# Kernel tuning notes

Hardware: AMD Instinct MI355X
Metric: run time of the kernel (lower is better)

The kernel has to match this reference:

```python
import jax, jax.numpy as jnp
import numpy as np

N, E, D = 100000, 1600000, 128
BN_EPS = 1e-5


def setup_inputs() -> dict:
    key = jax.random.key(0)
    k0, k1, k2 = jax.random.split(key, 3)
    x = jax.random.normal(k0, (N, D), dtype=jnp.float32)
    edge_index = jax.random.randint(k1, (2, E), 0, N, dtype=jnp.int32)
    # GCNConv weight (glorot-ish scale) and bias
    W = jax.random.normal(k2, (D, D), dtype=jnp.float32) * (1.0 / np.sqrt(D))
    b = jnp.zeros((D,), dtype=jnp.float32)
    # BatchNorm1d affine params
    gamma = jnp.ones((D,), dtype=jnp.float32)
    beta = jnp.zeros((D,), dtype=jnp.float32)
    # PReLU single shared slope (torch default init 0.25)
    a_prelu = jnp.asarray(0.25, dtype=jnp.float32)
    return {"x": x, "W": W, "b": b, "gamma": gamma, "beta": beta,
            "a_prelu": a_prelu, "edge_index": edge_index}


def reference(x, W, b, gamma, beta, a_prelu, edge_index):
    n = x.shape[0]
    loops = jnp.arange(n, dtype=edge_index.dtype)
    src = jnp.concatenate([edge_index[0], loops])  # [E+N]
    dst = jnp.concatenate([edge_index[1], loops])  # [E+N]

    # GCN symmetric normalization with self-loops: deg counts incoming edges
    deg = jax.ops.segment_sum(jnp.ones_like(dst, dtype=x.dtype), dst, num_segments=n)
    dinv = jax.lax.rsqrt(deg)  # deg >= 1 thanks to self-loops
    enorm = dinv[src] * dinv[dst]  # [E+N]

    xw = x @ W                                        # [N, D] transform first
    msg = xw[src] * enorm[:, None]                    # gather + scale
    out = jax.ops.segment_sum(msg, dst, num_segments=n) + b  # scatter-add

    # BatchNorm1d over nodes (training-mode batch statistics, biased var)
    mean = jnp.mean(out, axis=0)
    var = jnp.mean(jnp.square(out - mean), axis=0)
    out = (out - mean) * jax.lax.rsqrt(var + BN_EPS) * gamma + beta

    # PReLU (single shared slope); dropout is identity in eval mode
    out = jnp.where(out > 0, out, a_prelu * out)

    # identity residual (in_dim == out_dim)
    return out + x
```

## Files before the change

### kernel.cpp

```cpp
#include <hip/hip_runtime.h>

#define DIM 128
#define BSH 8
#define BUCK 256
#define CAP 6144
#define BINCH 1024
#define MAXB 1024
#define FPT 12

typedef __attribute__((ext_vector_type(8))) short bf16x8;
typedef __attribute__((ext_vector_type(4))) float f32x4;
union U8 { uint4 u; bf16x8 b; };

static __device__ __forceinline__ unsigned f2bf_bits(float f) {
  unsigned u = __float_as_uint(f);
  return (u + 0x7fffu + ((u >> 16) & 1u)) >> 16;
}
static __device__ __forceinline__ unsigned packbf(float a, float b) {
  return (f2bf_bits(a) & 0xffffu) | (f2bf_bits(b) << 16);
}
static __device__ __forceinline__ float bfu_lo(unsigned pk) { return __uint_as_float(pk << 16); }
static __device__ __forceinline__ float bfu_hi(unsigned pk) { return __uint_as_float(pk & 0xffff0000u); }

static __device__ __forceinline__ int eread(const int* __restrict__ e, long long idx, int fl64) {
  return fl64 ? e[idx * 2] : e[idx];
}

__global__ void k_probe(const int* __restrict__ eidx, int* __restrict__ iflag) {
  int lane = threadIdx.x;
  int w = eidx[lane * 2 + 1];
  unsigned long long m = __ballot(w == 0);
  if (lane == 0) *iflag = (__popcll(m) >= 48) ? 1 : 0;
}

__global__ __launch_bounds__(256) void k_prep(const int* __restrict__ eidx, int E,
                                              const int* __restrict__ iflag,
                                              int* __restrict__ bcnt,
                                              unsigned* __restrict__ tmp, int nbuck,
                                              const float* __restrict__ W,
                                              unsigned* __restrict__ wbt,
                                              int NBB) {
  __shared__ int hist[MAXB];
  __shared__ int lcur[MAXB];
  int bid = blockIdx.x;
  int tid = threadIdx.x;

  if (bid < NBB) {
    int fl = *iflag;
    long long ebase = (long long)bid * BINCH;
    for (int i = tid; i < nbuck; i += 256) hist[i] = 0;
    __syncthreads();
    unsigned pk[BINCH / 256];
    int bb[BINCH / 256];
#pragma unroll
    for (int it = 0; it < BINCH / 256; ++it) {
      long long e = ebase + it * 256 + tid;
      bb[it] = -1;
      if (e < E) {
        int s = eread(eidx, e, fl);
        int d = eread(eidx, (long long)E + e, fl);
        bb[it] = d >> BSH;
        pk[it] = ((unsigned)s << BSH) | (unsigned)(d & (BUCK - 1));
        atomicAdd(&hist[bb[it]], 1);
      }
    }
    __syncthreads();
    for (int b = tid; b < nbuck; b += 256) {
      int h = hist[b];
      lcur[b] = h ? atomicAdd(&bcnt[b], h) : 0;
    }
    __syncthreads();
#pragma unroll
    for (int it = 0; it < BINCH / 256; ++it) {
      if (bb[it] >= 0) {
        int sl = atomicAdd(&lcur[bb[it]], 1);
        if (sl < CAP) tmp[(unsigned)bb[it] * CAP + sl] = pk[it];
      }
    }
  } else {
    int w = (bid - NBB) * 256 + tid;
    int c = w >> 6, kk = w & 63;
    float lo = W[(unsigned)(2 * kk) * DIM + c];
    float hi = W[(unsigned)(2 * kk + 1) * DIM + c];
    wbt[(unsigned)c * 64 + kk] = packbf(lo, hi);
  }
}

__global__ __launch_bounds__(512) void k_fine(const int* __restrict__ bcnt,
                                              unsigned* __restrict__ tmp,
                                              int* __restrict__ ofs2,
                                              int* __restrict__ deg,
                                              float* __restrict__ dinv, int n) {
  __shared__ unsigned srt[CAP];
  __shared__ int hist[BUCK];
  __shared__ int sc[BUCK];
  __shared__ int lcur[BUCK];
  int b = blockIdx.x, tid = threadIdx.x;
  int cnt = bcnt[b];
  if (cnt > CAP) cnt = CAP;
  unsigned base = (unsigned)b * CAP;
  if (tid < BUCK) hist[tid] = 0;
  __syncthreads();
  unsigned r[FPT];
#pragma unroll
  for (int u = 0; u < FPT; ++u) {
    int j = u * 512 + tid;
    r[u] = 0xffffffffu;
    if (j < cnt) {
      r[u] = tmp[base + j];
      atomicAdd(&hist[r[u] & (BUCK - 1)], 1);
    }
  }
  __syncthreads();
  if (tid < 64) {
    int h0 = hist[tid * 4], h1 = hist[tid * 4 + 1];
    int h2 = hist[tid * 4 + 2], h3 = hist[tid * 4 + 3];
    int s = h0 + h1 + h2 + h3;
    int pre = s;
#pragma unroll
    for (int d = 1; d < 64; d <<= 1) {
      int t = __shfl_up(pre, d);
      if (tid >= d) pre += t;
    }
    pre -= s;
    int e0 = pre, e1 = pre + h0, e2 = e1 + h1, e3 = e2 + h2;
    sc[tid * 4] = e0;     lcur[tid * 4] = e0;
    sc[tid * 4 + 1] = e1; lcur[tid * 4 + 1] = e1;
    sc[tid * 4 + 2] = e2; lcur[tid * 4 + 2] = e2;
    sc[tid * 4 + 3] = e3; lcur[tid * 4 + 3] = e3;
  }
  __syncthreads();
#pragma unroll
  for (int u = 0; u < FPT; ++u) {
    if (r[u] != 0xffffffffu) {
      int sl = atomicAdd(&lcur[r[u] & (BUCK - 1)], 1);
      srt[sl] = r[u];
    }
  }
  __syncthreads();
#pragma unroll
  for (int u = 0; u < FPT; ++u) {
    int j = u * 512 + tid;
    if (j < cnt) tmp[base + j] = srt[j];
  }
  if (tid < BUCK) {
    int node = b * BUCK + tid;
    if (node < n) {
      int v = hist[tid];
      ofs2[node] = (int)base + sc[tid];
      deg[node] = v;
      dinv[node] = rsqrtf((float)(v + 1));
    }
  }
}

__global__ __launch_bounds__(256) void k_pack(const float* __restrict__ x,
                                              const float* __restrict__ dinv,
                                              unsigned* __restrict__ xb, int n) {
  int t = blockIdx.x * 256 + threadIdx.x;
  int i = t >> 6, p = t & 63;
  if (i >= n) return;
  float di = dinv[i];
  float2 v = *(const float2*)(x + (size_t)i * DIM + p * 2);
  xb[(unsigned)i * 64 + p] = packbf(v.x * di, v.y * di);
}

__global__ __launch_bounds__(256) void k_agg(const unsigned* __restrict__ xb,
                                             const unsigned* __restrict__ tmp,
                                             const int* __restrict__ ofs2,
                                             const int* __restrict__ deg,
                                             const float* __restrict__ dinv,
                                             unsigned* __restrict__ agg, int n) {
  int wid = blockIdx.x * 4 + (threadIdx.x >> 6);
  int lane = threadIdx.x & 63;
  if (wid >= n) return;
  float di = dinv[wid];
  unsigned xp = xb[(unsigned)wid * 64 + lane];
  float ax = bfu_lo(xp), ay = bfu_hi(xp);
  int e = __builtin_amdgcn_readfirstlane(ofs2[wid]);
  int e1 = e + __builtin_amdgcn_readfirstlane(deg[wid]);
  for (; e + 16 <= e1; e += 16) {
    unsigned s[16];
#pragma unroll
    for (int u = 0; u < 16; ++u) s[u] = tmp[(unsigned)(e + u)] >> BSH;
    unsigned v[16];
#pragma unroll
    for (int u = 0; u < 16; ++u) v[u] = xb[s[u] * 64 + lane];
#pragma unroll
    for (int u = 0; u < 16; ++u) { ax += bfu_lo(v[u]); ay += bfu_hi(v[u]); }
  }
  for (; e + 4 <= e1; e += 4) {
    unsigned s0 = tmp[(unsigned)e] >> BSH, s1 = tmp[(unsigned)e + 1] >> BSH;
    unsigned s2 = tmp[(unsigned)e + 2] >> BSH, s3 = tmp[(unsigned)e + 3] >> BSH;
    unsigned v0 = xb[s0 * 64 + lane], v1 = xb[s1 * 64 + lane];
    unsigned v2 = xb[s2 * 64 + lane], v3 = xb[s3 * 64 + lane];
    ax += bfu_lo(v0); ay += bfu_hi(v0);
    ax += bfu_lo(v1); ay += bfu_hi(v1);
    ax += bfu_lo(v2); ay += bfu_hi(v2);
    ax += bfu_lo(v3); ay += bfu_hi(v3);
  }
  for (; e < e1; ++e) {
    unsigned vv = xb[(tmp[(unsigned)e] >> BSH) * 64 + lane];
    ax += bfu_lo(vv); ay += bfu_hi(vv);
  }
  agg[(unsigned)wid * 64 + lane] = packbf(ax * di, ay * di);
}

__global__ __launch_bounds__(256) void k_gemm(
    const unsigned* __restrict__ agg, const unsigned* __restrict__ wbt,
    const float* __restrict__ bias, unsigned* __restrict__ preb,
    float* __restrict__ part, int n) {
  __shared__ unsigned SM[64 * 68 + 128 * 68];
  unsigned* As2 = SM;
  unsigned* WsT = SM + 64 * 68;
  int tid = threadIdx.x;
  int base = blockIdx.x * 64;

#pragma unroll
  for (int it = 0; it < 32; ++it) {
    int idx = it * 256 + tid;
    int c = idx >> 6, kk = idx & 63;
    WsT[c * 68 + kk] = wbt[idx];
  }
#pragma unroll
  for (int it = 0; it < 16; ++it) {
    int idx = it * 256 + tid;
    int rl = idx >> 6, c2 = idx & 63;
    int g = base + rl; if (g >= n) g = n - 1;
    As2[rl * 68 + c2] = agg[(unsigned)g * 64 + c2];
  }
  __syncthreads();

  int w = tid >> 6, l = tid & 63;
  int lg = l >> 4, lr = l & 15;
  f32x4 acc[8];
#pragma unroll
  for (int nt = 0; nt < 8; ++nt) acc[nt] = (f32x4){0.f, 0.f, 0.f, 0.f};

#pragma unroll
  for (int kt = 0; kt < 4; ++kt) {
    U8 bfr;
    bfr.u = *(const uint4*)&As2[(w * 16 + lr) * 68 + kt * 16 + lg * 4];
#pragma unroll
    for (int nt = 0; nt < 8; ++nt) {
      U8 afr;
      afr.u = *(const uint4*)&WsT[(nt * 16 + lr) * 68 + kt * 16 + lg * 4];
      acc[nt] = __builtin_amdgcn_mfma_f32_16x16x32_bf16(afr.b, bfr.b, acc[nt], 0, 0, 0);
    }
  }
  __syncthreads();

  float* Cf = (float*)SM;
#pragma unroll
  for (int nt = 0; nt < 8; ++nt) {
    *(f32x4*)&Cf[(w * 16 + lr) * 132 + nt * 16 + lg * 4] = acc[nt];
  }
  __syncthreads();

  float* bn = Cf + 64 * 132;
  int c2 = tid & 63, g4 = tid >> 6;
  float b0 = bias[2 * c2], b1 = bias[2 * c2 + 1];
  float cs0 = 0.f, cs1 = 0.f, cq0 = 0.f, cq1 = 0.f;
#pragma unroll
  for (int it = 0; it < 16; ++it) {
    int m = it * 4 + g4;
    int gg = base + m;
    float2 vv = *(const float2*)&Cf[m * 132 + 2 * c2];
    float v0 = vv.x + b0, v1 = vv.y + b1;
    if (gg < n) {
      preb[(unsigned)gg * 64 + c2] = packbf(v0, v1);
      cs0 += v0; cq0 += v0 * v0;
      cs1 += v1; cq1 += v1 * v1;
    }
  }
  bn[g4 * 256 + 2 * c2] = cs0;
  bn[g4 * 256 + 2 * c2 + 1] = cs1;
  bn[g4 * 256 + 128 + 2 * c2] = cq0;
  bn[g4 * 256 + 128 + 2 * c2 + 1] = cq1;
  __syncthreads();
  part[(size_t)blockIdx.x * 256 + tid] = bn[tid] + bn[256 + tid] + bn[512 + tid] + bn[768 + tid];
}

__global__ __launch_bounds__(256) void k_redbn(const float* __restrict__ part, int nb,
                                               const float* __restrict__ gma,
                                               const float* __restrict__ bta,
                                               float* __restrict__ sc_,
                                               float* __restrict__ sh_, float invn) {
  __shared__ float r1[256], r2[256];
  int c = blockIdx.x, t = threadIdx.x;
  float s = 0.f, q = 0.f;
  for (int i = t; i < nb; i += 256) {
    s += part[(size_t)i * 256 + c];
    q += part[(size_t)i * 256 + 128 + c];
  }
  r1[t] = s; r2[t] = q;
  __syncthreads();
  for (int k = 128; k > 0; k >>= 1) {
    if (t < k) { r1[t] += r1[t + k]; r2[t] += r2[t + k]; }
    __syncthreads();
  }
  if (t == 0) {
    float mean = r1[0] * invn;
    float var = r2[0] * invn - mean * mean;
    float inv = rsqrtf(var + 1e-5f);
    float g = gma[c] * inv;
    sc_[c] = g;
    sh_[c] = bta[c] - mean * g;
  }
}

__global__ __launch_bounds__(256) void k_final(const unsigned* __restrict__ preb,
                                               const float* __restrict__ x,
                                               const float* __restrict__ sc,
                                               const float* __restrict__ sh,
                                               const float* __restrict__ apre,
                                               float* __restrict__ out, int n) {
  int t = blockIdx.x * 256 + threadIdx.x;
  int i = t >> 6, p = t & 63;
  if (i >= n) return;
  float a = apre[0];
  int c = p * 2;
  unsigned pk = preb[(unsigned)i * 64 + p];
  float t0 = bfu_lo(pk) * sc[c] + sh[c];
  float t1 = bfu_hi(pk) * sc[c + 1] + sh[c + 1];
  t0 = t0 > 0.f ? t0 : a * t0;
  t1 = t1 > 0.f ? t1 : a * t1;
  float2 xv = *(const float2*)(x + (size_t)i * DIM + c);
  t0 += xv.x;
  t1 += xv.y;
  *(float2*)(out + (size_t)i * DIM + c) = make_float2(t0, t1);
}

extern "C" void kernel_launch(void* const* d_in, const int* in_sizes, int n_in,
                              void* d_out, int out_size, void* d_ws, size_t ws_size,
                              hipStream_t stream) {
  (void)n_in; (void)out_size; (void)ws_size;
  const float* x    = (const float*)d_in[0];
  const float* W    = (const float*)d_in[1];
  const float* b    = (const float*)d_in[2];
  const float* gma  = (const float*)d_in[3];
  const float* bta  = (const float*)d_in[4];
  const float* apre = (const float*)d_in[5];
  const int* eidx   = (const int*)d_in[6];
  float* out        = (float*)d_out;

  const int N = in_sizes[0] / DIM;
  const int E = in_sizes[6] / 2;
  const int NB = (N + 63) / 64;
  const int NBUCK = (N + BUCK - 1) / BUCK;
  const int NBB = (E + BINCH - 1) / BINCH;
  const int NWT = 32;

  char* wsb = (char*)d_ws;
  size_t off_b = 0;
  auto take = [&](size_t bytes) -> void* {
    void* p = wsb + off_b;
    off_b += (bytes + 255) & ~(size_t)255;
    return p;
  };
  int*      iflag = (int*)     take(256);
  int*      deg   = (int*)     take((size_t)N * 4);
  int*      bcnt  = (int*)     take((size_t)NBUCK * 4);
  int*      ofs2  = (int*)     take((size_t)N * 4);
  float*    dinv  = (float*)   take((size_t)N * 4);
  unsigned* wbt   = (unsigned*)take((size_t)DIM * 64 * 4);
  unsigned* tmp   = (unsigned*)take((size_t)NBUCK * CAP * 4);
  unsigned* xb    = (unsigned*)take((size_t)N * 64 * 4);
  unsigned* agg   = (unsigned*)take((size_t)N * 64 * 4);
  float*    part  = (float*)   take((size_t)NB * 256 * 4);
  float*    sc    = (float*)   take(DIM * 4);
  float*    sh    = (float*)   take(DIM * 4);
  unsigned* preb  = agg;

  hipMemsetAsync(bcnt, 0, (size_t)NBUCK * 4, stream);

  k_probe <<<1, 64, 0, stream>>>(eidx, iflag);
  k_prep  <<<NBB + NWT, 256, 0, stream>>>(eidx, E, iflag, bcnt, tmp, NBUCK, W, wbt, NBB);
  k_fine  <<<NBUCK, 512, 0, stream>>>(bcnt, tmp, ofs2, deg, dinv, N);
  k_pack  <<<(N * 64 + 255) / 256, 256, 0, stream>>>(x, dinv, xb, N);
  k_agg   <<<(N + 3) / 4, 256, 0, stream>>>(xb, tmp, ofs2, deg, dinv, agg, N);
  k_gemm  <<<NB, 256, 0, stream>>>(agg, wbt, b, preb, part, N);
  k_redbn <<<DIM, 256, 0, stream>>>(part, NB, gma, bta, sc, sh, 1.0f / (float)N);
  k_final <<<(N * 64 + 255) / 256, 256, 0, stream>>>(preb, x, sc, sh, apre, out, N);
}
```

Baseline: 280.2 us.

## Fuse per-bucket sort with aggregation and compute degrees via global atomics

Degree counting moves to a separate atomic k_deg kernel so the bf16 x packing can be merged into the k_prep launch. The per-bucket counting sort is fused with neighbor aggregation in one 1024-thread block per bucket, which reads sorted sources directly from shared memory. This removes the write-back of sorted tmp and the separate ofs2/deg/dinv arrays, and BINCH is doubled. In exchange it adds a pass of global atomics over E edges and gives only NBUCK (~391) large blocks to the gather-heavy aggregation, which may underutilize the GPU and hurt latency hiding.

```diff
diff --git a/kernel.cpp b/kernel.cpp
--- a/kernel.cpp
+++ b/kernel.cpp
@@ -4,9 +4,8 @@
 #define BSH 8
 #define BUCK 256
 #define CAP 6144
-#define BINCH 1024
+#define BINCH 2048
 #define MAXB 1024
-#define FPT 12
 
 typedef __attribute__((ext_vector_type(8))) short bf16x8;
 typedef __attribute__((ext_vector_type(4))) float f32x4;
@@ -31,6 +30,16 @@
   int w = eidx[lane * 2 + 1];
   unsigned long long m = __ballot(w == 0);
   if (lane == 0) *iflag = (__popcll(m) >= 48) ? 1 : 0;
+}
+
+__global__ __launch_bounds__(256) void k_deg(const int* __restrict__ eidx, int E,
+                                             const int* __restrict__ iflag,
+                                             int* __restrict__ deg) {
+  int e = blockIdx.x * 256 + threadIdx.x;
+  if (e >= E) return;
+  int fl = *iflag;
+  int d = eread(eidx, (long long)E + e, fl);
+  atomicAdd(&deg[d], 1);
 }
 
 __global__ __launch_bounds__(256) void k_prep(const int* __restrict__ eidx, int E,
@@ -39,7 +48,10 @@
                                               unsigned* __restrict__ tmp, int nbuck,
                                               const float* __restrict__ W,
                                               unsigned* __restrict__ wbt,
-                                              int NBB) {
+                                              const float* __restrict__ x,
+                                              const int* __restrict__ deg,
+                                              unsigned* __restrict__ xb, int n,
+                                              int NBB, int NWT) {
   __shared__ int hist[MAXB];
   __shared__ int lcur[MAXB];
   int bid = blockIdx.x;
@@ -77,23 +89,29 @@
         if (sl < CAP) tmp[(unsigned)bb[it] * CAP + sl] = pk[it];
       }
     }
-  } else {
+  } else if (bid < NBB + NWT) {
     int w = (bid - NBB) * 256 + tid;
     int c = w >> 6, kk = w & 63;
     float lo = W[(unsigned)(2 * kk) * DIM + c];
     float hi = W[(unsigned)(2 * kk + 1) * DIM + c];
     wbt[(unsigned)c * 64 + kk] = packbf(lo, hi);
-  }
-}
-
-__global__ __launch_bounds__(512) void k_fine(const int* __restrict__ bcnt,
-                                              unsigned* __restrict__ tmp,
-                                              int* __restrict__ ofs2,
-                                              int* __restrict__ deg,
-                                              float* __restrict__ dinv, int n) {
+  } else {
+    int t = (bid - NBB - NWT) * 256 + tid;
+    int i = t >> 6, p = t & 63;
+    if (i >= n) return;
+    float di = rsqrtf((float)(deg[i] + 1));
+    float2 v = *(const float2*)(x + (size_t)i * DIM + p * 2);
+    xb[(unsigned)i * 64 + p] = packbf(v.x * di, v.y * di);
+  }
+}
+
+__global__ __launch_bounds__(1024) void k_fagg(const int* __restrict__ bcnt,
+                                               const unsigned* __restrict__ tmp,
+                                               const unsigned* __restrict__ xb,
+                                               unsigned* __restrict__ agg, int n) {
   __shared__ unsigned srt[CAP];
   __shared__ int hist[BUCK];
-  __shared__ int sc[BUCK];
+  __shared__ int sc2[BUCK];
   __shared__ int lcur[BUCK];
   int b = blockIdx.x, tid = threadIdx.x;
   int cnt = bcnt[b];
@@ -101,10 +119,10 @@
   unsigned base = (unsigned)b * CAP;
   if (tid < BUCK) hist[tid] = 0;
   __syncthreads();
-  unsigned r[FPT];
-#pragma unroll
-  for (int u = 0; u < FPT; ++u) {
-    int j = u * 512 + tid;
+  unsigned r[CAP / 1024];
+#pragma unroll
+  for (int u = 0; u < CAP / 1024; ++u) {
+    int j = u * 1024 + tid;
     r[u] = 0xffffffffu;
     if (j < cnt) {
       r[u] = tmp[base + j];
@@ -124,86 +142,59 @@
     }
     pre -= s;
     int e0 = pre, e1 = pre + h0, e2 = e1 + h1, e3 = e2 + h2;
-    sc[tid * 4] = e0;     lcur[tid * 4] = e0;
-    sc[tid * 4 + 1] = e1; lcur[tid * 4 + 1] = e1;
-    sc[tid * 4 + 2] = e2; lcur[tid * 4 + 2] = e2;
-    sc[tid * 4 + 3] = e3; lcur[tid * 4 + 3] = e3;
-  }
-  __syncthreads();
-#pragma unroll
-  for (int u = 0; u < FPT; ++u) {
+    sc2[tid * 4] = e0;     lcur[tid * 4] = e0;
+    sc2[tid * 4 + 1] = e1; lcur[tid * 4 + 1] = e1;
+    sc2[tid * 4 + 2] = e2; lcur[tid * 4 + 2] = e2;
+    sc2[tid * 4 + 3] = e3; lcur[tid * 4 + 3] = e3;
+  }
+  __syncthreads();
+#pragma unroll
+  for (int u = 0; u < CAP / 1024; ++u) {
     if (r[u] != 0xffffffffu) {
       int sl = atomicAdd(&lcur[r[u] & (BUCK - 1)], 1);
       srt[sl] = r[u];
     }
   }
   __syncthreads();
-#pragma unroll
-  for (int u = 0; u < FPT; ++u) {
-    int j = u * 512 + tid;
-    if (j < cnt) tmp[base + j] = srt[j];
-  }
-  if (tid < BUCK) {
-    int node = b * BUCK + tid;
-    if (node < n) {
-      int v = hist[tid];
-      ofs2[node] = (int)base + sc[tid];
-      deg[node] = v;
-      dinv[node] = rsqrtf((float)(v + 1));
-    }
-  }
-}
-
-__global__ __launch_bounds__(256) void k_pack(const float* __restrict__ x,
-                                              const float* __restrict__ dinv,
-                                              unsigned* __restrict__ xb, int n) {
-  int t = blockIdx.x * 256 + threadIdx.x;
-  int i = t >> 6, p = t & 63;
-  if (i >= n) return;
-  float di = dinv[i];
-  float2 v = *(const float2*)(x + (size_t)i * DIM + p * 2);
-  xb[(unsigned)i * 64 + p] = packbf(v.x * di, v.y * di);
-}
-
-__global__ __launch_bounds__(256) void k_agg(const unsigned* __restrict__ xb,
-                                             const unsigned* __restrict__ tmp,
-                                             const int* __restrict__ ofs2,
-                                             const int* __restrict__ deg,
-                                             const float* __restrict__ dinv,
-                                             unsigned* __restrict__ agg, int n) {
-  int wid = blockIdx.x * 4 + (threadIdx.x >> 6);
-  int lane = threadIdx.x & 63;
-  if (wid >= n) return;
-  float di = dinv[wid];
-  unsigned xp = xb[(unsigned)wid * 64 + lane];
-  float ax = bfu_lo(xp), ay = bfu_hi(xp);
-  int e = __builtin_amdgcn_readfirstlane(ofs2[wid]);
-  int e1 = e + __builtin_amdgcn_readfirstlane(deg[wid]);
-  for (; e + 16 <= e1; e += 16) {
-    unsigned s[16];
-#pragma unroll
-    for (int u = 0; u < 16; ++u) s[u] = tmp[(unsigned)(e + u)] >> BSH;
-    unsigned v[16];
-#pragma unroll
-    for (int u = 0; u < 16; ++u) v[u] = xb[s[u] * 64 + lane];
-#pragma unroll
-    for (int u = 0; u < 16; ++u) { ax += bfu_lo(v[u]); ay += bfu_hi(v[u]); }
-  }
-  for (; e + 4 <= e1; e += 4) {
-    unsigned s0 = tmp[(unsigned)e] >> BSH, s1 = tmp[(unsigned)e + 1] >> BSH;
-    unsigned s2 = tmp[(unsigned)e + 2] >> BSH, s3 = tmp[(unsigned)e + 3] >> BSH;
-    unsigned v0 = xb[s0 * 64 + lane], v1 = xb[s1 * 64 + lane];
-    unsigned v2 = xb[s2 * 64 + lane], v3 = xb[s3 * 64 + lane];
-    ax += bfu_lo(v0); ay += bfu_hi(v0);
-    ax += bfu_lo(v1); ay += bfu_hi(v1);
-    ax += bfu_lo(v2); ay += bfu_hi(v2);
-    ax += bfu_lo(v3); ay += bfu_hi(v3);
-  }
-  for (; e < e1; ++e) {
-    unsigned vv = xb[(tmp[(unsigned)e] >> BSH) * 64 + lane];
-    ax += bfu_lo(vv); ay += bfu_hi(vv);
-  }
-  agg[(unsigned)wid * 64 + lane] = packbf(ax * di, ay * di);
+  int wv = tid >> 6, lane = tid & 63;
+  for (int ln = wv; ln < BUCK; ln += 16) {
+    int node = b * BUCK + ln;
+    if (node >= n) break;
+    int o = sc2[ln], dg = hist[ln];
+    float di = rsqrtf((float)(dg + 1));
+    unsigned xp = xb[(unsigned)node * 64 + lane];
+    float ax = bfu_lo(xp), ay = bfu_hi(xp);
+    int j = o, je = o + dg;
+    for (; j + 8 <= je; j += 8) {
+      unsigned s0 = srt[j] >> BSH, s1 = srt[j + 1] >> BSH;
+      unsigned s2 = srt[j + 2] >> BSH, s3 = srt[j + 3] >> BSH;
+      unsigned s4 = srt[j + 4] >> BSH, s5 = srt[j + 5] >> BSH;
+      unsigned s6 = srt[j + 6] >> BSH, s7 = srt[j + 7] >> BSH;
+      unsigned v0 = xb[s0 * 64 + lane], v1 = xb[s1 * 64 + lane];
+      unsigned v2 = xb[s2 * 64 + lane], v3 = xb[s3 * 64 + lane];
+      unsigned v4 = xb[s4 * 64 + lane], v5 = xb[s5 * 64 + lane];
+      unsigned v6 = xb[s6 * 64 + lane], v7 = xb[s7 * 64 + lane];
+      ax += bfu_lo(v0); ay += bfu_hi(v0);
+      ax += bfu_lo(v1); ay += bfu_hi(v1);
+      ax += bfu_lo(v2); ay += bfu_hi(v2);
+      ax += bfu_lo(v3); ay += bfu_hi(v3);
+      ax += bfu_lo(v4); ay += bfu_hi(v4);
+      ax += bfu_lo(v5); ay += bfu_hi(v5);
+      ax += bfu_lo(v6); ay += bfu_hi(v6);
+      ax += bfu_lo(v7); ay += bfu_hi(v7);
+    }
+    for (; j + 2 <= je; j += 2) {
+      unsigned s0 = srt[j] >> BSH, s1 = srt[j + 1] >> BSH;
+      unsigned v0 = xb[s0 * 64 + lane], v1 = xb[s1 * 64 + lane];
+      ax += bfu_lo(v0); ay += bfu_hi(v0);
+      ax += bfu_lo(v1); ay += bfu_hi(v1);
+    }
+    if (j < je) {
+      unsigned vv = xb[(srt[j] >> BSH) * 64 + lane];
+      ax += bfu_lo(vv); ay += bfu_hi(vv);
+    }
+    agg[(unsigned)node * 64 + lane] = packbf(ax * di, ay * di);
+  }
 }
 
 __global__ __launch_bounds__(256) void k_gemm(
@@ -350,6 +341,7 @@
   const int NBUCK = (N + BUCK - 1) / BUCK;
   const int NBB = (E + BINCH - 1) / BINCH;
   const int NWT = 32;
+  const int NPK = (N * 64 + 255) / 256;
 
   char* wsb = (char*)d_ws;
   size_t off_b = 0;
@@ -359,10 +351,8 @@
     return p;
   };
   int*      iflag = (int*)     take(256);
-  int*      deg   = (int*)     take((size_t)N * 4);
-  int*      bcnt  = (int*)     take((size_t)NBUCK * 4);
-  int*      ofs2  = (int*)     take((size_t)N * 4);
-  float*    dinv  = (float*)   take((size_t)N * 4);
+  int*      deg   = (int*)     take((size_t)(N + NBUCK) * 4);
+  int*      bcnt  = deg + N;
   unsigned* wbt   = (unsigned*)take((size_t)DIM * 64 * 4);
   unsigned* tmp   = (unsigned*)take((size_t)NBUCK * CAP * 4);
   unsigned* xb    = (unsigned*)take((size_t)N * 64 * 4);
@@ -372,13 +362,13 @@
   float*    sh    = (float*)   take(DIM * 4);
   unsigned* preb  = agg;
 
-  hipMemsetAsync(bcnt, 0, (size_t)NBUCK * 4, stream);
+  hipMemsetAsync(deg, 0, (size_t)(N + NBUCK) * 4, stream);
 
   k_probe <<<1, 64, 0, stream>>>(eidx, iflag);
-  k_prep  <<<NBB + NWT, 256, 0, stream>>>(eidx, E, iflag, bcnt, tmp, NBUCK, W, wbt, NBB);
-  k_fine  <<<NBUCK, 512, 0, stream>>>(bcnt, tmp, ofs2, deg, dinv, N);
-  k_pack  <<<(N * 64 + 255) / 256, 256, 0, stream>>>(x, dinv, xb, N);
-  k_agg   <<<(N + 3) / 4, 256, 0, stream>>>(xb, tmp, ofs2, deg, dinv, agg, N);
+  k_deg   <<<(E + 255) / 256, 256, 0, stream>>>(eidx, E, iflag, deg);
+  k_prep  <<<NBB + NWT + NPK, 256, 0, stream>>>(eidx, E, iflag, bcnt, tmp, NBUCK,
+                                                W, wbt, x, deg, xb, N, NBB, NWT);
+  k_fagg  <<<NBUCK, 1024, 0, stream>>>(bcnt, tmp, xb, agg, N);
   k_gemm  <<<NB, 256, 0, stream>>>(agg, wbt, b, preb, part, N);
   k_redbn <<<DIM, 256, 0, stream>>>(part, NB, gma, bta, sc, sh, 1.0f / (float)N);
   k_final <<<(N * 64 + 255) / 256, 256, 0, stream>>>(preb, x, sc, sh, apre, out, N);
```

Result: slower. 319.7 us (+14.1%).

## Fuse probe into prep and x packing into bucket sort; drop dinv buffer

Applied to the files above, without the earlier changes.

Folds the index-width probe into every k_prep block and moves the x-to-bf16 scaled packing into the per-bucket sort kernel, using degrees held in shared memory. The dinv array goes away, and k_agg recomputes rsqrt from deg. BINCH is doubled, so each prep block bins twice as many edges. This removes two launches and one global round trip for dinv, but each prep block now re-reads the probe slice, and the sort kernel does more serial work per block.

```diff
diff --git a/kernel.cpp b/kernel.cpp
--- a/kernel.cpp
+++ b/kernel.cpp
@@ -3,8 +3,8 @@
 #define DIM 128
 #define BSH 8
 #define BUCK 256
-#define CAP 6144
-#define BINCH 1024
+#define CAP2 6144
+#define BINCH 2048
 #define MAXB 1024
 #define FPT 12
 
@@ -26,30 +26,28 @@
   return fl64 ? e[idx * 2] : e[idx];
 }
 
-__global__ void k_probe(const int* __restrict__ eidx, int* __restrict__ iflag) {
-  int lane = threadIdx.x;
-  int w = eidx[lane * 2 + 1];
-  unsigned long long m = __ballot(w == 0);
-  if (lane == 0) *iflag = (__popcll(m) >= 48) ? 1 : 0;
-}
-
 __global__ __launch_bounds__(256) void k_prep(const int* __restrict__ eidx, int E,
-                                              const int* __restrict__ iflag,
                                               int* __restrict__ bcnt,
-                                              unsigned* __restrict__ tmp, int nbuck,
+                                              unsigned* __restrict__ tmp2, int nbuck,
                                               const float* __restrict__ W,
                                               unsigned* __restrict__ wbt,
                                               int NBB) {
   __shared__ int hist[MAXB];
   __shared__ int lcur[MAXB];
+  __shared__ int sfl;
   int bid = blockIdx.x;
   int tid = threadIdx.x;
 
   if (bid < NBB) {
-    int fl = *iflag;
-    long long ebase = (long long)bid * BINCH;
+    if (tid < 64) {
+      int w = eidx[tid * 2 + 1];
+      unsigned long long m = __ballot(w == 0);
+      if (tid == 0) sfl = (__popcll(m) >= 48) ? 1 : 0;
+    }
     for (int i = tid; i < nbuck; i += 256) hist[i] = 0;
     __syncthreads();
+    int fl = sfl;
+    long long ebase = (long long)bid * BINCH;
     unsigned pk[BINCH / 256];
     int bb[BINCH / 256];
 #pragma unroll
@@ -74,7 +72,7 @@
     for (int it = 0; it < BINCH / 256; ++it) {
       if (bb[it] >= 0) {
         int sl = atomicAdd(&lcur[bb[it]], 1);
-        if (sl < CAP) tmp[(unsigned)bb[it] * CAP + sl] = pk[it];
+        if (sl < CAP2) tmp2[(unsigned)bb[it] * CAP2 + sl] = pk[it];
       }
     }
   } else {
@@ -86,19 +84,21 @@
   }
 }
 
-__global__ __launch_bounds__(512) void k_fine(const int* __restrict__ bcnt,
-                                              unsigned* __restrict__ tmp,
-                                              int* __restrict__ ofs2,
-                                              int* __restrict__ deg,
-                                              float* __restrict__ dinv, int n) {
-  __shared__ unsigned srt[CAP];
+__global__ __launch_bounds__(512) void k_histsort(const int* __restrict__ bcnt,
+                                                  unsigned* __restrict__ tmp2,
+                                                  int* __restrict__ ofs2,
+                                                  int* __restrict__ deg,
+                                                  const float* __restrict__ x,
+                                                  unsigned* __restrict__ xb, int n) {
+  __shared__ unsigned srt[CAP2];
   __shared__ int hist[BUCK];
-  __shared__ int sc[BUCK];
+  __shared__ int sc2[BUCK];
   __shared__ int lcur[BUCK];
+  __shared__ float dls[BUCK];
   int b = blockIdx.x, tid = threadIdx.x;
   int cnt = bcnt[b];
-  if (cnt > CAP) cnt = CAP;
-  unsigned base = (unsigned)b * CAP;
+  if (cnt > CAP2) cnt = CAP2;
+  unsigned base = (unsigned)b * CAP2;
   if (tid < BUCK) hist[tid] = 0;
   __syncthreads();
   unsigned r[FPT];
@@ -107,7 +107,7 @@
     int j = u * 512 + tid;
     r[u] = 0xffffffffu;
     if (j < cnt) {
-      r[u] = tmp[base + j];
+      r[u] = tmp2[base + j];
       atomicAdd(&hist[r[u] & (BUCK - 1)], 1);
     }
   }
@@ -124,10 +124,10 @@
     }
     pre -= s;
     int e0 = pre, e1 = pre + h0, e2 = e1 + h1, e3 = e2 + h2;
-    sc[tid * 4] = e0;     lcur[tid * 4] = e0;
-    sc[tid * 4 + 1] = e1; lcur[tid * 4 + 1] = e1;
-    sc[tid * 4 + 2] = e2; lcur[tid * 4 + 2] = e2;
-    sc[tid * 4 + 3] = e3; lcur[tid * 4 + 3] = e3;
+    sc2[tid * 4] = e0;     lcur[tid * 4] = e0;
+    sc2[tid * 4 + 1] = e1; lcur[tid * 4 + 1] = e1;
+    sc2[tid * 4 + 2] = e2; lcur[tid * 4 + 2] = e2;
+    sc2[tid * 4 + 3] = e3; lcur[tid * 4 + 3] = e3;
   }
   __syncthreads();
 #pragma unroll
@@ -137,52 +137,52 @@
       srt[sl] = r[u];
     }
   }
+  if (tid < BUCK) dls[tid] = rsqrtf((float)(hist[tid] + 1));
   __syncthreads();
 #pragma unroll
   for (int u = 0; u < FPT; ++u) {
     int j = u * 512 + tid;
-    if (j < cnt) tmp[base + j] = srt[j];
+    if (j < cnt) tmp2[base + j] = srt[j];
   }
   if (tid < BUCK) {
     int node = b * BUCK + tid;
     if (node < n) {
-      int v = hist[tid];
-      ofs2[node] = (int)base + sc[tid];
-      deg[node] = v;
-      dinv[node] = rsqrtf((float)(v + 1));
-    }
-  }
-}
-
-__global__ __launch_bounds__(256) void k_pack(const float* __restrict__ x,
-                                              const float* __restrict__ dinv,
-                                              unsigned* __restrict__ xb, int n) {
-  int t = blockIdx.x * 256 + threadIdx.x;
-  int i = t >> 6, p = t & 63;
-  if (i >= n) return;
-  float di = dinv[i];
-  float2 v = *(const float2*)(x + (size_t)i * DIM + p * 2);
-  xb[(unsigned)i * 64 + p] = packbf(v.x * di, v.y * di);
-}
-
-__global__ __launch_bounds__(256) void k_agg(const unsigned* __restrict__ xb,
-                                             const unsigned* __restrict__ tmp,
+      ofs2[node] = (int)base + sc2[tid];
+      deg[node] = hist[tid];
+    }
+  }
+  int nb0 = b * BUCK;
+#pragma unroll
+  for (int it = 0; it < 32; ++it) {
+    int idx = it * 512 + tid;
+    int ln = idx >> 6, p = idx & 63;
+    int node = nb0 + ln;
+    if (node < n) {
+      float di = dls[ln];
+      float2 v = *(const float2*)(x + (size_t)node * DIM + p * 2);
+      xb[(unsigned)node * 64 + p] = packbf(v.x * di, v.y * di);
+    }
+  }
+}
+
+__global__ __launch_bounds__(256) void k_agg(const unsigned* __restrict__ tmp2,
+                                             const unsigned* __restrict__ xb,
                                              const int* __restrict__ ofs2,
                                              const int* __restrict__ deg,
-                                             const float* __restrict__ dinv,
                                              unsigned* __restrict__ agg, int n) {
   int wid = blockIdx.x * 4 + (threadIdx.x >> 6);
   int lane = threadIdx.x & 63;
   if (wid >= n) return;
-  float di = dinv[wid];
+  int dg = __builtin_amdgcn_readfirstlane(deg[wid]);
+  float di = rsqrtf((float)(dg + 1));
   unsigned xp = xb[(unsigned)wid * 64 + lane];
   float ax = bfu_lo(xp), ay = bfu_hi(xp);
   int e = __builtin_amdgcn_readfirstlane(ofs2[wid]);
-  int e1 = e + __builtin_amdgcn_readfirstlane(deg[wid]);
+  int e1 = e + dg;
   for (; e + 16 <= e1; e += 16) {
     unsigned s[16];
 #pragma unroll
-    for (int u = 0; u < 16; ++u) s[u] = tmp[(unsigned)(e + u)] >> BSH;
+    for (int u = 0; u < 16; ++u) s[u] = tmp2[(unsigned)(e + u)] >> BSH;
     unsigned v[16];
 #pragma unroll
     for (int u = 0; u < 16; ++u) v[u] = xb[s[u] * 64 + lane];
@@ -190,8 +190,8 @@
     for (int u = 0; u < 16; ++u) { ax += bfu_lo(v[u]); ay += bfu_hi(v[u]); }
   }
   for (; e + 4 <= e1; e += 4) {
-    unsigned s0 = tmp[(unsigned)e] >> BSH, s1 = tmp[(unsigned)e + 1] >> BSH;
-    unsigned s2 = tmp[(unsigned)e + 2] >> BSH, s3 = tmp[(unsigned)e + 3] >> BSH;
+    unsigned s0 = tmp2[(unsigned)e] >> BSH, s1 = tmp2[(unsigned)e + 1] >> BSH;
+    unsigned s2 = tmp2[(unsigned)e + 2] >> BSH, s3 = tmp2[(unsigned)e + 3] >> BSH;
     unsigned v0 = xb[s0 * 64 + lane], v1 = xb[s1 * 64 + lane];
     unsigned v2 = xb[s2 * 64 + lane], v3 = xb[s3 * 64 + lane];
     ax += bfu_lo(v0); ay += bfu_hi(v0);
@@ -200,7 +200,7 @@
     ax += bfu_lo(v3); ay += bfu_hi(v3);
   }
   for (; e < e1; ++e) {
-    unsigned vv = xb[(tmp[(unsigned)e] >> BSH) * 64 + lane];
+    unsigned vv = xb[(tmp2[(unsigned)e] >> BSH) * 64 + lane];
     ax += bfu_lo(vv); ay += bfu_hi(vv);
   }
   agg[(unsigned)wid * 64 + lane] = packbf(ax * di, ay * di);
@@ -347,7 +347,7 @@
   const int N = in_sizes[0] / DIM;
   const int E = in_sizes[6] / 2;
   const int NB = (N + 63) / 64;
-  const int NBUCK = (N + BUCK - 1) / BUCK;
+  const int NBUCK = (N + BUCK - 1) >> BSH;
   const int NBB = (E + BINCH - 1) / BINCH;
   const int NWT = 32;
 
@@ -358,13 +358,11 @@
     off_b += (bytes + 255) & ~(size_t)255;
     return p;
   };
-  int*      iflag = (int*)     take(256);
-  int*      deg   = (int*)     take((size_t)N * 4);
   int*      bcnt  = (int*)     take((size_t)NBUCK * 4);
   int*      ofs2  = (int*)     take((size_t)N * 4);
-  float*    dinv  = (float*)   take((size_t)N * 4);
+  int*      deg   = (int*)     take((size_t)N * 4);
   unsigned* wbt   = (unsigned*)take((size_t)DIM * 64 * 4);
-  unsigned* tmp   = (unsigned*)take((size_t)NBUCK * CAP * 4);
+  unsigned* tmp2  = (unsigned*)take((size_t)NBUCK * CAP2 * 4);
   unsigned* xb    = (unsigned*)take((size_t)N * 64 * 4);
   unsigned* agg   = (unsigned*)take((size_t)N * 64 * 4);
   float*    part  = (float*)   take((size_t)NB * 256 * 4);
@@ -374,12 +372,10 @@
 
   hipMemsetAsync(bcnt, 0, (size_t)NBUCK * 4, stream);
 
-  k_probe <<<1, 64, 0, stream>>>(eidx, iflag);
-  k_prep  <<<NBB + NWT, 256, 0, stream>>>(eidx, E, iflag, bcnt, tmp, NBUCK, W, wbt, NBB);
-  k_fine  <<<NBUCK, 512, 0, stream>>>(bcnt, tmp, ofs2, deg, dinv, N);
-  k_pack  <<<(N * 64 + 255) / 256, 256, 0, stream>>>(x, dinv, xb, N);
-  k_agg   <<<(N + 3) / 4, 256, 0, stream>>>(xb, tmp, ofs2, deg, dinv, agg, N);
-  k_gemm  <<<NB, 256, 0, stream>>>(agg, wbt, b, preb, part, N);
-  k_redbn <<<DIM, 256, 0, stream>>>(part, NB, gma, bta, sc, sh, 1.0f / (float)N);
-  k_final <<<(N * 64 + 255) / 256, 256, 0, stream>>>(preb, x, sc, sh, apre, out, N);
-}
+  k_prep     <<<NBB + NWT, 256, 0, stream>>>(eidx, E, bcnt, tmp2, NBUCK, W, wbt, NBB);
+  k_histsort <<<NBUCK, 512, 0, stream>>>(bcnt, tmp2, ofs2, deg, x, xb, N);
+  k_agg      <<<(N + 3) / 4, 256, 0, stream>>>(tmp2, xb, ofs2, deg, agg, N);
+  k_gemm     <<<NB, 256, 0, stream>>>(agg, wbt, b, preb, part, N);
+  k_redbn    <<<DIM, 256, 0, stream>>>(part, NB, gma, bta, sc, sh, 1.0f / (float)N);
+  k_final    <<<(N * 64 + 255) / 256, 256, 0, stream>>>(preb, x, sc, sh, apre, out, N);
+}
```

Result: faster. 271.8 us (-3.0%).
